# Kernel tuning notes

Hardware: AMD Instinct MI355X
Metric: run time of the kernel (lower is better)

## Reference

```python
import jax, jax.numpy as jnp
import numpy as np
from jax import lax

EPS = 1e-5

def layernorm_c(x, w, b):
    # WithBias LayerNorm over channel dim per spatial location (Restormer style)
    mu = jnp.mean(x, axis=1, keepdims=True)
    var = jnp.var(x, axis=1, keepdims=True)  # population variance (unbiased=False)
    xn = (x - mu) / jnp.sqrt(var + EPS)
    return xn * w[None, :, None, None] + b[None, :, None, None]

def conv1x1(x, w, b):
    # w: (C_out, C_in)
    y = jnp.einsum('bchw,oc->bohw', x, w)
    return y + b[None, :, None, None]

def dwconv3x3(x, w, b):
    # w: (C, 1, 3, 3), depthwise
    y = lax.conv_general_dilated(x, w, window_strides=(1, 1), padding=((1, 1), (1, 1)),
                                 dimension_numbers=('NCHW', 'OIHW', 'NCHW'),
                                 feature_group_count=x.shape[1])
    return y + b[None, :, None, None]

def to_patches(x, p):
    B, C, H, W = x.shape
    x = x.reshape(B, C, H // p, p, W // p, p)
    return x.transpose(0, 1, 2, 4, 3, 5)  # (B,C,h,w,p,p)

def from_patches(x):
    B, C, h, w, p1, p2 = x.shape
    return x.transpose(0, 1, 2, 4, 3, 5).reshape(B, C, h * p1, w * p2)

def setup_inputs() -> dict:
    key = jax.random.key(0)
    ks = jax.random.split(key, 12)
    B, C, H, W = 8, 128, 192, 192
    s = 0.05
    return {
        'x': jax.random.normal(ks[0], (B, C, H, W), jnp.float32),
        'evt': jax.random.normal(ks[1], (B, C, H, W), jnp.float32),
        'ln_img_w': jnp.ones((C,), jnp.float32),
        'ln_img_b': jnp.zeros((C,), jnp.float32),
        'ln_evt_w': jnp.ones((C,), jnp.float32),
        'ln_evt_b': jnp.zeros((C,), jnp.float32),
        'q_w': jax.random.normal(ks[2], (2 * C, C), jnp.float32) * s,
        'q_b': jnp.zeros((2 * C,), jnp.float32),
        'q_dw_w': jax.random.normal(ks[3], (2 * C, 1, 3, 3), jnp.float32) * s,
        'q_dw_b': jnp.zeros((2 * C,), jnp.float32),
        'kv_w': jax.random.normal(ks[4], (4 * C, C), jnp.float32) * s,
        'kv_b': jnp.zeros((4 * C,), jnp.float32),
        'kv_dw_w': jax.random.normal(ks[5], (4 * C, 1, 3, 3), jnp.float32) * s,
        'kv_dw_b': jnp.zeros((4 * C,), jnp.float32),
        'ln_corr_w': jnp.ones((2 * C,), jnp.float32),
        'ln_corr_b': jnp.zeros((2 * C,), jnp.float32),
        'proj_w': jax.random.normal(ks[6], (C, 2 * C), jnp.float32) * s,
        'proj_b': jnp.zeros((C,), jnp.float32),
    }

def reference(x, evt, ln_img_w, ln_img_b, ln_evt_w, ln_evt_b,
              q_w, q_b, q_dw_w, q_dw_b, kv_w, kv_b, kv_dw_w, kv_dw_b,
              ln_corr_w, ln_corr_b, proj_w, proj_b):
    p = 8
    C = x.shape[1]
    xn = layernorm_c(x, ln_img_w, ln_img_b)
    en = layernorm_c(evt, ln_evt_w, ln_evt_b)
    q = dwconv3x3(conv1x1(xn, q_w, q_b), q_dw_w, q_dw_b)          # (B,2C,H,W)
    kv = dwconv3x3(conv1x1(en, kv_w, kv_b), kv_dw_w, kv_dw_b)      # (B,4C,H,W)
    k, v = kv[:, :2 * C], kv[:, 2 * C:]
    q_p = to_patches(q, p)  # (B,2C,h,w,p,p)
    k_p = to_patches(k, p)
    corr = jnp.fft.irfft2(jnp.fft.rfft2(q_p.astype(jnp.float32)) *
                          jnp.fft.rfft2(k_p.astype(jnp.float32)), s=(p, p))
    corr = from_patches(corr)                                      # (B,2C,H,W)
    corr = layernorm_c(corr, ln_corr_w, ln_corr_b)
    return conv1x1(v * corr, proj_w, proj_b)
```

## Files before the change

kernel.cpp:

```cpp
#include <hip/hip_runtime.h>
#include <stdint.h>

#define BATCH 8
#define CIN   128
#define HH    192
#define WW    192
#define HW    (HH*WW)
#define PXB   576
#define CH    2
#define RS    216

typedef _Float16 half_t;
typedef _Float16 f16x8 __attribute__((ext_vector_type(8)));
typedef _Float16 f16x4 __attribute__((ext_vector_type(4)));
typedef _Float16 f16x2 __attribute__((ext_vector_type(2)));
typedef float    f32x4 __attribute__((ext_vector_type(4)));
typedef float    f32x16 __attribute__((ext_vector_type(16)));
typedef unsigned int u32;

__device__ __forceinline__ float DOT2(u32 a, u32 b, float c) {
#if __has_builtin(__builtin_amdgcn_fdot2)
    return __builtin_amdgcn_fdot2(__builtin_bit_cast(f16x2, a),
                                  __builtin_bit_cast(f16x2, b), c, false);
#else
    f16x2 av = __builtin_bit_cast(f16x2, a), bv = __builtin_bit_cast(f16x2, b);
    return c + (float)av[0] * (float)bv[0] + (float)av[1] * (float)bv[1];
#endif
}

#define SMEM_BYTES 52736
#define WSH_OFF    17408
#define MU_OFF     52224

__global__ __launch_bounds__(256)
void wcvt_kernel(const float* __restrict__ qw, const float* __restrict__ kvw,
                 const float* __restrict__ pw, const float* __restrict__ qdw,
                 const float* __restrict__ kvdw, half_t* __restrict__ out)
{
    int q = blockIdx.x * 256 + threadIdx.x;
    if (q >= 34496) return;
    int idx = q * 4;
    const float* src;
    int off;
    if (idx < 32768)       { src = qw;   off = idx; }
    else if (idx < 98304)  { src = kvw;  off = idx - 32768; }
    else if (idx < 131072) { src = pw;   off = idx - 98304; }
    else if (idx < 133376) { src = qdw;  off = idx - 131072; }
    else                   { src = kvdw; off = idx - 133376; }
    float4 v = *(const float4*)&src[off];
    f16x4 o = { (half_t)v.x, (half_t)v.y, (half_t)v.z, (half_t)v.w };
    *(f16x4*)&out[idx] = o;
}

template<int OC>
__global__ __launch_bounds__(256)
void ln_gemm_kernel(const float* __restrict__ x,
                    const float* __restrict__ lnw, const float* __restrict__ lnb,
                    const half_t* __restrict__ wf16, const float* __restrict__ wb,
                    half_t* __restrict__ out)
{
    __shared__ __attribute__((aligned(16))) char smem[SMEM_BYTES];
    half_t (*As)[136]  = (half_t(*)[136])smem;
    half_t (*Wsh)[136] = (half_t(*)[136])(smem + WSH_OFF);
    float  (*Cst)[68]  = (float (*)[68]) (smem + WSH_OFF);
    float* redA = (float*)(smem + WSH_OFF);
    float* redB = (float*)(smem + WSH_OFF + 4096);
    float* mu_s = (float*)(smem + MU_OFF);
    float* rs_s = mu_s + 64;

    const int tid  = threadIdx.x;
    const int l    = tid & 63;
    const int w    = tid >> 6;
    const int lrow = l & 31;
    const int lk   = (l >> 5) * 8;

    const long p0  = (long)blockIdx.x * 64;
    const int  b   = (int)(p0 / HW);
    const int  hw0 = (int)(p0 - (long)b * HW);

    const int pxq = tid & 15;
    const int cg  = tid >> 4;
    const float* xb = x + (size_t)b * CIN * HW + hw0 + pxq * 4;
    float4 vals[8];
    float4 s1 = {0.f,0.f,0.f,0.f}, s2 = {0.f,0.f,0.f,0.f};
#pragma unroll
    for (int j = 0; j < 8; ++j) {
        float4 vv = *(const float4*)&xb[(size_t)(cg * 8 + j) * HW];
        vals[j] = vv;
        s1.x += vv.x; s1.y += vv.y; s1.z += vv.z; s1.w += vv.w;
        s2.x += vv.x*vv.x; s2.y += vv.y*vv.y; s2.z += vv.z*vv.z; s2.w += vv.w*vv.w;
    }
    redA[cg * 64 + pxq * 4 + 0] = s1.x; redB[cg * 64 + pxq * 4 + 0] = s2.x;
    redA[cg * 64 + pxq * 4 + 1] = s1.y; redB[cg * 64 + pxq * 4 + 1] = s2.y;
    redA[cg * 64 + pxq * 4 + 2] = s1.z; redB[cg * 64 + pxq * 4 + 2] = s2.z;
    redA[cg * 64 + pxq * 4 + 3] = s1.w; redB[cg * 64 + pxq * 4 + 3] = s2.w;
    __syncthreads();
    if (tid < 64) {
        float su = 0.f, sq = 0.f;
#pragma unroll
        for (int c = 0; c < 16; ++c) { su += redA[c * 64 + tid]; sq += redB[c * 64 + tid]; }
        float mu  = su * (1.f / 128.f);
        float var = sq * (1.f / 128.f) - mu * mu;
        mu_s[tid] = mu;
        rs_s[tid] = rsqrtf(var + 1e-5f);
    }
    __syncthreads();
    {
        float mu_a[4], rs_a[4];
#pragma unroll
        for (int k = 0; k < 4; ++k) { mu_a[k] = mu_s[pxq * 4 + k]; rs_a[k] = rs_s[pxq * 4 + k]; }
#pragma unroll
        for (int k = 0; k < 4; ++k) {
            f16x8 o;
#pragma unroll
            for (int j = 0; j < 8; ++j) {
                int c = cg * 8 + j;
                float v = (k == 0) ? vals[j].x : (k == 1) ? vals[j].y
                        : (k == 2) ? vals[j].z : vals[j].w;
                o[j] = (half_t)((v - mu_a[k]) * rs_a[k] * lnw[c] + lnb[c]);
            }
            *(f16x8*)&As[pxq * 4 + k][cg * 8] = o;
        }
    }

    for (int nc = 0; nc < OC / 128; ++nc) {
        const int n0 = nc * 128;
        if (nc) __syncthreads();
#pragma unroll
        for (int i = 0; i < 8; ++i) {
            int f  = i * 256 + tid;
            int n  = f >> 4;
            int xh = (f & 15) * 8;
            *(f16x8*)&Wsh[n][xh] = *(const f16x8*)&wf16[(size_t)(n0 + n) * CIN + xh];
        }
        __syncthreads();

        f16x8 af[8];
#pragma unroll
        for (int kk = 0; kk < 8; ++kk)
            af[kk] = *(const f16x8*)&Wsh[w * 32 + lrow][kk * 16 + lk];

        f32x16 acc0, acc1;
#pragma unroll
        for (int i = 0; i < 16; ++i) { acc0[i] = 0.f; acc1[i] = 0.f; }
#pragma unroll
        for (int kk = 0; kk < 8; ++kk) {
            f16x8 b0 = *(const f16x8*)&As[lrow][kk * 16 + lk];
            f16x8 b1 = *(const f16x8*)&As[32 + lrow][kk * 16 + lk];
            acc0 = __builtin_amdgcn_mfma_f32_32x32x16_f16(af[kk], b0, acc0, 0, 0, 0);
            acc1 = __builtin_amdgcn_mfma_f32_32x32x16_f16(af[kk], b1, acc1, 0, 0, 0);
        }
        __syncthreads();

#pragma unroll
        for (int r = 0; r < 16; ++r) {
            int oc = w * 32 + (r & 3) + 8 * (r >> 2) + 4 * (l >> 5);
            Cst[oc][lrow]      = acc0[r];
            Cst[oc][32 + lrow] = acc1[r];
        }
        __syncthreads();

#pragma unroll
        for (int i = 0; i < 4; ++i) {
            int idx = i * 256 + tid;
            int oc  = idx >> 3;
            int pxg = idx & 7;
            const float4 a = *(const float4*)&Cst[oc][pxg * 8];
            const float4 c = *(const float4*)&Cst[oc][pxg * 8 + 4];
            float bias = wb[n0 + oc];
            f16x8 o = { (half_t)(a.x + bias), (half_t)(a.y + bias),
                        (half_t)(a.z + bias), (half_t)(a.w + bias),
                        (half_t)(c.x + bias), (half_t)(c.y + bias),
                        (half_t)(c.z + bias), (half_t)(c.w + bias) };
            *(f16x8*)&out[((size_t)b * OC + n0 + oc) * HW + hw0 + pxg * 8] = o;
        }
    }
}

__global__ __launch_bounds__(256)
void corr_strip_kernel(const half_t* __restrict__ q1, const half_t* __restrict__ kv1,
                       const half_t* __restrict__ qdw16, const float* __restrict__ qb,
                       const half_t* __restrict__ kdw16, const float* __restrict__ kb,
                       half_t* __restrict__ corr, half_t* __restrict__ vd)
{
    __shared__ __attribute__((aligned(16))) half_t raw[6][10][RS];
    __shared__ __attribute__((aligned(16))) half_t qd[2][8][RS];
    __shared__ __attribute__((aligned(16))) half_t krev[2][8][RS];

    const int bid = blockIdx.x;
    const int cg  = bid & 127;
    const int ph  = (bid >> 7) % 24;
    const int lb  = (bid >> 7) / 24;
    const int c0  = cg * CH;
    const int tid = threadIdx.x;

    if (tid < 120) {
        int side = tid & 1;
        int row  = (tid >> 1) % 10;
        int a    = tid / 20;
        f16x8 z = {};
        *(f16x8*)&raw[a][row][side ? 200 : 0] = z;
    }

    for (int i = 0; i < 6; ++i) {
        int idx = tid + 256 * i;
        if (idx >= 1440) break;
        int vec = idx % 24;
        int row = (idx / 24) % 10;
        int a   = idx / 240;
        int ch  = a & 1;
        int gh  = ph * 8 - 1 + row;
        f16x8 v = {};
        if (gh >= 0 && gh < HH) {
            const half_t* src;
            if (a < 2)      src = q1  + ((size_t)lb * 256 + c0 + ch) * HW;
            else if (a < 4) src = kv1 + ((size_t)lb * 512 + c0 + ch) * HW;
            else            src = kv1 + ((size_t)lb * 512 + 256 + c0 + ch) * HW;
            v = *(const f16x8*)&src[(size_t)gh * WW + vec * 8];
        }
        *(f16x8*)&raw[a][row][8 + vec * 8] = v;
    }
    __syncthreads();

    for (int i = 0; i < 3; ++i) {
        int unit = tid + 256 * i;
        if (unit >= 576) break;
        int u   = unit & 7;
        int xg2 = (unit >> 3) % 12;
        int a   = unit / 96;
        int ch  = a & 1;
        const half_t (*rw)[RS] = raw[a];
        const half_t* wt;
        float bias;
        if (a < 2)      { wt = qdw16 + (size_t)(c0 + ch) * 9;       bias = qb[c0 + ch]; }
        else if (a < 4) { wt = kdw16 + (size_t)(c0 + ch) * 9;       bias = kb[c0 + ch]; }
        else            { wt = kdw16 + (size_t)(256 + c0 + ch) * 9; bias = kb[256 + c0 + ch]; }
        u32 w01[3], w2z[3];
#pragma unroll
        for (int dy = 0; dy < 3; ++dy) {
            u32 a0 = (u32)__builtin_bit_cast(unsigned short, wt[dy * 3 + 0]);
            u32 a1 = (u32)__builtin_bit_cast(unsigned short, wt[dy * 3 + 1]);
            u32 a2 = (u32)__builtin_bit_cast(unsigned short, wt[dy * 3 + 2]);
            w01[dy] = a0 | (a1 << 16);
            w2z[dy] = a2;
        }
        const int x0 = xg2 * 16;
        float acc[16];
#pragma unroll
        for (int xx = 0; xx < 16; ++xx) acc[xx] = bias;
#pragma unroll
        for (int dy = 0; dy < 3; ++dy) {
            const half_t* rowp = &rw[u + dy][x0];
            uint4 c0v = *(const uint4*)(rowp);
            uint4 c1v = *(const uint4*)(rowp + 8);
            uint4 c2v = *(const uint4*)(rowp + 16);
            uint4 c3v = *(const uint4*)(rowp + 24);
            u32 H[13] = {c0v.x,c0v.y,c0v.z,c0v.w, c1v.x,c1v.y,c1v.z,c1v.w,
                         c2v.x,c2v.y,c2v.z,c2v.w, c3v.x};
            u32 A[12];
#pragma unroll
            for (int m = 3; m < 12; ++m) A[m] = (H[m] >> 16) | (H[m + 1] << 16);
#pragma unroll
            for (int xx = 0; xx < 16; ++xx) {
                u32 p01 = (xx & 1) ? H[(7 + xx) >> 1] : A[3 + (xx >> 1)];
                u32 p2  = (xx & 1) ? H[(9 + xx) >> 1] : A[4 + (xx >> 1)];
                acc[xx] = DOT2(p01, w01[dy], acc[xx]);
                acc[xx] = DOT2(p2,  w2z[dy], acc[xx]);
            }
        }
        f16x8 o0, o1;
#pragma unroll
        for (int xx = 0; xx < 8; ++xx) { o0[xx] = (half_t)acc[xx]; o1[xx] = (half_t)acc[8 + xx]; }
        if (a < 2) {
            *(f16x8*)&qd[ch][u][x0]     = o0;
            *(f16x8*)&qd[ch][u][x0 + 8] = o1;
        } else if (a < 4) {
            f16x8 r0v, r1v;
            r0v[0] = (half_t)acc[0];
            r1v[0] = (half_t)acc[8];
#pragma unroll
            for (int j = 1; j < 8; ++j) {
                r0v[j] = (half_t)acc[8 - j];
                r1v[j] = (half_t)acc[16 - j];
            }
            *(f16x8*)&krev[ch][u][x0]     = r0v;
            *(f16x8*)&krev[ch][u][x0 + 8] = r1v;
        } else {
            half_t* dst = &vd[((size_t)lb * 256 + c0 + ch) * HW + (size_t)(ph * 8 + u) * WW + x0];
            *(f16x8*)dst       = o0;
            *(f16x8*)(dst + 8) = o1;
        }
    }
    __syncthreads();

    for (int i = 0; i < 2; ++i) {
        int unit = tid + 256 * i;
        if (unit >= 384) break;
        int c   = unit / 192;
        int rem = unit % 192;
        int pw  = rem >> 3;
        int u   = rem & 7;
        float acc[8];
#pragma unroll
        for (int v = 0; v < 8; ++v) acc[v] = 0.f;
#pragma unroll
        for (int s = 0; s < 8; ++s) {
            int r = (u - s) & 7;
            uint4 q4 = *(const uint4*)&qd[c][s][pw * 8];
            uint4 k4 = *(const uint4*)&krev[c][r][pw * 8];
            u32 Q[4] = {q4.x, q4.y, q4.z, q4.w};
            u32 K[4] = {k4.x, k4.y, k4.z, k4.w};
            u32 S[4];
#pragma unroll
            for (int m = 0; m < 4; ++m) S[m] = (K[m] >> 16) | (K[(m + 1) & 3] << 16);
#pragma unroll
            for (int v = 0; v < 8; ++v) {
                const int o = 8 - v;
#pragma unroll
                for (int tt = 0; tt < 4; ++tt) {
                    u32 pr = (o & 1) ? S[(((o - 1) >> 1) + tt) & 3]
                                     : K[((o >> 1) + tt) & 3];
                    acc[v] = DOT2(Q[tt], pr, acc[v]);
                }
            }
        }
        f16x8 ov;
#pragma unroll
        for (int v = 0; v < 8; ++v) ov[v] = (half_t)acc[v];
        *(f16x8*)&corr[((size_t)lb * 256 + c0 + c) * HW + (size_t)(ph * 8 + u) * WW + pw * 8] = ov;
    }
}

__global__ __launch_bounds__(256)
void proj_kernel(const half_t* __restrict__ corr, const half_t* __restrict__ vd,
                 const float* __restrict__ lnw, const float* __restrict__ lnb,
                 const half_t* __restrict__ wp16, const float* __restrict__ wb,
                 float* __restrict__ out)
{
    __shared__ __attribute__((aligned(16))) char smem[SMEM_BYTES];
    half_t (*As)[136]  = (half_t(*)[136])smem;
    half_t (*Wsh)[136] = (half_t(*)[136])(smem + WSH_OFF);
    float  (*Cst)[68]  = (float (*)[68]) (smem + WSH_OFF);
    float* redA = (float*)(smem + WSH_OFF);
    float* redB = (float*)(smem + WSH_OFF + 8192);
    float* mu_s = (float*)(smem + MU_OFF);
    float* rs_s = mu_s + 64;

    const int tid  = threadIdx.x;
    const int l    = tid & 63;
    const int w    = tid >> 6;
    const int lrow = l & 31;
    const int lk   = (l >> 5) * 8;

    const long p0  = (long)blockIdx.x * 64;
    const int  lb  = (int)(p0 / HW);
    const int  hw0 = (int)(p0 - (long)lb * HW);

    const int pxq8 = tid & 7;
    const int cg   = tid >> 3;
    const half_t* cb = corr + (size_t)lb * 256 * HW + hw0 + pxq8 * 8;
    const half_t* vb = vd   + (size_t)lb * 256 * HW + hw0 + pxq8 * 8;

    f16x8 cpk[8];
    float s1[8], s2[8];
#pragma unroll
    for (int p = 0; p < 8; ++p) { s1[p] = 0.f; s2[p] = 0.f; }
#pragma unroll
    for (int j = 0; j < 8; ++j) {
        cpk[j] = *(const f16x8*)&cb[(size_t)(cg * 8 + j) * HW];
#pragma unroll
        for (int p = 0; p < 8; ++p) {
            float f = (float)cpk[j][p];
            s1[p] += f; s2[p] += f * f;
        }
    }
#pragma unroll
    for (int p = 0; p < 8; ++p) {
        redA[cg * 64 + pxq8 * 8 + p] = s1[p];
        redB[cg * 64 + pxq8 * 8 + p] = s2[p];
    }
    __syncthreads();
    if (tid < 64) {
        float su = 0.f, sq = 0.f;
#pragma unroll
        for (int c = 0; c < 32; ++c) { su += redA[c * 64 + tid]; sq += redB[c * 64 + tid]; }
        float mu  = su * (1.f / 256.f);
        float var = sq * (1.f / 256.f) - mu * mu;
        mu_s[tid] = mu;
        rs_s[tid] = rsqrtf(var + 1e-5f);
    }
    __syncthreads();

    f32x16 acc0, acc1;
#pragma unroll
    for (int i = 0; i < 16; ++i) { acc0[i] = 0.f; acc1[i] = 0.f; }

    for (int kc = 0; kc < 2; ++kc) {
        if (kc) __syncthreads();
        if ((cg >> 4) == kc) {
            const int cgl = cg & 15;
            float mu8[8], rs8[8];
#pragma unroll
            for (int p = 0; p < 8; ++p) {
                mu8[p] = mu_s[pxq8 * 8 + p];
                rs8[p] = rs_s[pxq8 * 8 + p];
            }
            f16x8 vvv[8];
            float lw[8], lbv[8];
#pragma unroll
            for (int j = 0; j < 8; ++j) {
                int c = kc * 128 + cgl * 8 + j;
                vvv[j] = *(const f16x8*)&vb[(size_t)c * HW];
                lw[j]  = lnw[c]; lbv[j] = lnb[c];
            }
#pragma unroll
            for (int p = 0; p < 8; ++p) {
                f16x8 o;
#pragma unroll
                for (int j = 0; j < 8; ++j) {
                    float cf = (float)cpk[j][p];
                    o[j] = (half_t)(((cf - mu8[p]) * rs8[p] * lw[j] + lbv[j]) * (float)vvv[j][p]);
                }
                *(f16x8*)&As[pxq8 * 8 + p][cgl * 8] = o;
            }
        }
#pragma unroll
        for (int i = 0; i < 8; ++i) {
            int f  = i * 256 + tid;
            int n  = f >> 4;
            int xh = (f & 15) * 8;
            *(f16x8*)&Wsh[n][xh] = *(const f16x8*)&wp16[(size_t)n * 256 + kc * 128 + xh];
        }
        __syncthreads();

        f16x8 af[8];
#pragma unroll
        for (int kk = 0; kk < 8; ++kk)
            af[kk] = *(const f16x8*)&Wsh[w * 32 + lrow][kk * 16 + lk];
#pragma unroll
        for (int kk = 0; kk < 8; ++kk) {
            f16x8 b0 = *(const f16x8*)&As[lrow][kk * 16 + lk];
            f16x8 b1 = *(const f16x8*)&As[32 + lrow][kk * 16 + lk];
            acc0 = __builtin_amdgcn_mfma_f32_32x32x16_f16(af[kk], b0, acc0, 0, 0, 0);
            acc1 = __builtin_amdgcn_mfma_f32_32x32x16_f16(af[kk], b1, acc1, 0, 0, 0);
        }
    }
    __syncthreads();

#pragma unroll
    for (int r = 0; r < 16; ++r) {
        int oc = w * 32 + (r & 3) + 8 * (r >> 2) + 4 * (l >> 5);
        Cst[oc][lrow]      = acc0[r];
        Cst[oc][32 + lrow] = acc1[r];
    }
    __syncthreads();

#pragma unroll
    for (int i = 0; i < 8; ++i) {
        int idx = i * 256 + tid;
        int oc  = idx >> 4;
        int pxq = idx & 15;
        float4 a = *(const float4*)&Cst[oc][pxq * 4];
        float bias = wb[oc];
        a.x += bias; a.y += bias; a.z += bias; a.w += bias;
        *(float4*)&out[((size_t)lb * 128 + oc) * HW + hw0 + pxq * 4] = a;
    }
}

extern "C" void kernel_launch(void* const* d_in, const int* in_sizes, int n_in,
                              void* d_out, int out_size, void* d_ws, size_t ws_size,
                              hipStream_t stream)
{
    const float* x        = (const float*)d_in[0];
    const float* evt      = (const float*)d_in[1];
    const float* ln_img_w = (const float*)d_in[2];
    const float* ln_img_b = (const float*)d_in[3];
    const float* ln_evt_w = (const float*)d_in[4];
    const float* ln_evt_b = (const float*)d_in[5];
    const float* q_w      = (const float*)d_in[6];
    const float* q_b      = (const float*)d_in[7];
    const float* q_dw_w   = (const float*)d_in[8];
    const float* q_dw_b   = (const float*)d_in[9];
    const float* kv_w     = (const float*)d_in[10];
    const float* kv_b     = (const float*)d_in[11];
    const float* kv_dw_w  = (const float*)d_in[12];
    const float* kv_dw_b  = (const float*)d_in[13];
    const float* ln_corr_w= (const float*)d_in[14];
    const float* ln_corr_b= (const float*)d_in[15];
    const float* proj_w   = (const float*)d_in[16];
    const float* proj_b   = (const float*)d_in[17];
    float* out = (float*)d_out;

    const size_t wtail = (ws_size - 278528) & ~(size_t)255;
    half_t* wf    = (half_t*)((char*)d_ws + wtail);
    half_t* wq16  = wf;
    half_t* wkv16 = wf + 32768;
    half_t* wp16  = wf + 98304;
    half_t* qdw16 = wf + 131072;
    half_t* kdw16 = wf + 133376;

    const size_t per_b = (size_t)(256 + 512 + 256 + 256) * HW * sizeof(half_t);
    int PB = 1;
    if      (wtail >= 8 * per_b) PB = 8;
    else if (wtail >= 4 * per_b) PB = 4;
    else if (wtail >= 2 * per_b) PB = 2;

    half_t* q1   = (half_t*)d_ws;
    half_t* kv1  = q1  + (size_t)PB * 256 * HW;
    half_t* vd   = kv1 + (size_t)PB * 512 * HW;
    half_t* corr = vd  + (size_t)PB * 256 * HW;

    dim3 blk(256);
    wcvt_kernel<<<135, blk, 0, stream>>>(q_w, kv_w, proj_w, q_dw_w, kv_dw_w, wf);

    for (int b0 = 0; b0 < BATCH; b0 += PB) {
        int nb = PB;
        ln_gemm_kernel<256><<<nb * PXB, blk, 0, stream>>>(
            x + (size_t)b0 * CIN * HW, ln_img_w, ln_img_b, wq16, q_b, q1);
        ln_gemm_kernel<512><<<nb * PXB, blk, 0, stream>>>(
            evt + (size_t)b0 * CIN * HW, ln_evt_w, ln_evt_b, wkv16, kv_b, kv1);
        corr_strip_kernel<<<nb * 24 * 128, blk, 0, stream>>>(
            q1, kv1, qdw16, q_dw_b, kdw16, kv_dw_b, corr, vd);
        proj_kernel<<<nb * PXB, blk, 0, stream>>>(
            corr, vd, ln_corr_w, ln_corr_b, wp16, proj_b,
            out + (size_t)b0 * 128 * HW);
    }
}
```

Baseline: 650.9 us.

## Merge q/kv LN-GEMMs and overlap projection with next-chunk LN-GEMM

The two LayerNorm+1x1-conv kernels are refactored into device bodies and launched together as one interleaved-block kernel, so q and kv are computed in a single launch. When the batch is processed in chunks, the projection for the current chunk and the LN-GEMMs for the next chunk are dispatched in the same grid. This is meant to cut launch count and fill the GPU during kernel tails by co-scheduling independent work. In exchange, the LN-GEMM output-channel count becomes a runtime value, which may cost some unrolling, and the heterogeneous blocks can raise register and LDS pressure.

```diff
diff --git a/kernel.cpp b/kernel.cpp
--- a/kernel.cpp
+++ b/kernel.cpp
@@ -52,14 +52,12 @@
     *(f16x4*)&out[idx] = o;
 }
 
-template<int OC>
-__global__ __launch_bounds__(256)
-void ln_gemm_kernel(const float* __restrict__ x,
-                    const float* __restrict__ lnw, const float* __restrict__ lnb,
-                    const half_t* __restrict__ wf16, const float* __restrict__ wb,
-                    half_t* __restrict__ out)
-{
-    __shared__ __attribute__((aligned(16))) char smem[SMEM_BYTES];
+__device__ void ln_gemm_body(char* smem, int bid, int OC,
+    const float* __restrict__ x,
+    const float* __restrict__ lnw, const float* __restrict__ lnb,
+    const half_t* __restrict__ wf16, const float* __restrict__ wb,
+    half_t* __restrict__ out)
+{
     half_t (*As)[136]  = (half_t(*)[136])smem;
     half_t (*Wsh)[136] = (half_t(*)[136])(smem + WSH_OFF);
     float  (*Cst)[68]  = (float (*)[68]) (smem + WSH_OFF);
@@ -74,9 +72,8 @@
     const int lrow = l & 31;
     const int lk   = (l >> 5) * 8;
 
-    const long p0  = (long)blockIdx.x * 64;
-    const int  b   = (int)(p0 / HW);
-    const int  hw0 = (int)(p0 - (long)b * HW);
+    const int b   = bid / PXB;
+    const int hw0 = (bid - b * PXB) * 64;
 
     const int pxq = tid & 15;
     const int cg  = tid >> 4;
@@ -123,7 +120,7 @@
         }
     }
 
-    for (int nc = 0; nc < OC / 128; ++nc) {
+    for (int nc = 0; nc < (OC >> 7); ++nc) {
         const int n0 = nc * 128;
         if (nc) __syncthreads();
 #pragma unroll
@@ -175,6 +172,193 @@
             *(f16x8*)&out[((size_t)b * OC + n0 + oc) * HW + hw0 + pxg * 8] = o;
         }
     }
+}
+
+__device__ void proj_body(char* smem, int bid,
+    const half_t* __restrict__ corr, const half_t* __restrict__ vd,
+    const float* __restrict__ lnw, const float* __restrict__ lnb,
+    const half_t* __restrict__ wp16, const float* __restrict__ wb,
+    float* __restrict__ out)
+{
+    half_t (*As)[136]  = (half_t(*)[136])smem;
+    half_t (*Wsh)[136] = (half_t(*)[136])(smem + WSH_OFF);
+    float  (*Cst)[68]  = (float (*)[68]) (smem + WSH_OFF);
+    float* redA = (float*)(smem + WSH_OFF);
+    float* redB = (float*)(smem + WSH_OFF + 8192);
+    float* mu_s = (float*)(smem + MU_OFF);
+    float* rs_s = mu_s + 64;
+
+    const int tid  = threadIdx.x;
+    const int l    = tid & 63;
+    const int w    = tid >> 6;
+    const int lrow = l & 31;
+    const int lk   = (l >> 5) * 8;
+
+    const int lb  = bid / PXB;
+    const int hw0 = (bid - lb * PXB) * 64;
+
+    const int pxq8 = tid & 7;
+    const int cg   = tid >> 3;
+    const half_t* cb = corr + (size_t)lb * 256 * HW + hw0 + pxq8 * 8;
+    const half_t* vb = vd   + (size_t)lb * 256 * HW + hw0 + pxq8 * 8;
+
+    f16x8 cpk[8];
+    float s1[8], s2[8];
+#pragma unroll
+    for (int p = 0; p < 8; ++p) { s1[p] = 0.f; s2[p] = 0.f; }
+#pragma unroll
+    for (int j = 0; j < 8; ++j) {
+        cpk[j] = *(const f16x8*)&cb[(size_t)(cg * 8 + j) * HW];
+#pragma unroll
+        for (int p = 0; p < 8; ++p) {
+            float f = (float)cpk[j][p];
+            s1[p] += f; s2[p] += f * f;
+        }
+    }
+#pragma unroll
+    for (int p = 0; p < 8; ++p) {
+        redA[cg * 64 + pxq8 * 8 + p] = s1[p];
+        redB[cg * 64 + pxq8 * 8 + p] = s2[p];
+    }
+    __syncthreads();
+    if (tid < 64) {
+        float su = 0.f, sq = 0.f;
+#pragma unroll
+        for (int c = 0; c < 32; ++c) { su += redA[c * 64 + tid]; sq += redB[c * 64 + tid]; }
+        float mu  = su * (1.f / 256.f);
+        float var = sq * (1.f / 256.f) - mu * mu;
+        mu_s[tid] = mu;
+        rs_s[tid] = rsqrtf(var + 1e-5f);
+    }
+    __syncthreads();
+
+    f32x16 acc0, acc1;
+#pragma unroll
+    for (int i = 0; i < 16; ++i) { acc0[i] = 0.f; acc1[i] = 0.f; }
+
+    for (int kc = 0; kc < 2; ++kc) {
+        if (kc) __syncthreads();
+        if ((cg >> 4) == kc) {
+            const int cgl = cg & 15;
+            float mu8[8], rs8[8];
+#pragma unroll
+            for (int p = 0; p < 8; ++p) {
+                mu8[p] = mu_s[pxq8 * 8 + p];
+                rs8[p] = rs_s[pxq8 * 8 + p];
+            }
+            f16x8 vvv[8];
+            float lw[8], lbv[8];
+#pragma unroll
+            for (int j = 0; j < 8; ++j) {
+                int c = kc * 128 + cgl * 8 + j;
+                vvv[j] = *(const f16x8*)&vb[(size_t)c * HW];
+                lw[j]  = lnw[c]; lbv[j] = lnb[c];
+            }
+#pragma unroll
+            for (int p = 0; p < 8; ++p) {
+                f16x8 o;
+#pragma unroll
+                for (int j = 0; j < 8; ++j) {
+                    float cf = (float)cpk[j][p];
+                    o[j] = (half_t)(((cf - mu8[p]) * rs8[p] * lw[j] + lbv[j]) * (float)vvv[j][p]);
+                }
+                *(f16x8*)&As[pxq8 * 8 + p][cgl * 8] = o;
+            }
+        }
+#pragma unroll
+        for (int i = 0; i < 8; ++i) {
+            int f  = i * 256 + tid;
+            int n  = f >> 4;
+            int xh = (f & 15) * 8;
+            *(f16x8*)&Wsh[n][xh] = *(const f16x8*)&wp16[(size_t)n * 256 + kc * 128 + xh];
+        }
+        __syncthreads();
+
+        f16x8 af[8];
+#pragma unroll
+        for (int kk = 0; kk < 8; ++kk)
+            af[kk] = *(const f16x8*)&Wsh[w * 32 + lrow][kk * 16 + lk];
+#pragma unroll
+        for (int kk = 0; kk < 8; ++kk) {
+            f16x8 b0 = *(const f16x8*)&As[lrow][kk * 16 + lk];
+            f16x8 b1 = *(const f16x8*)&As[32 + lrow][kk * 16 + lk];
+            acc0 = __builtin_amdgcn_mfma_f32_32x32x16_f16(af[kk], b0, acc0, 0, 0, 0);
+            acc1 = __builtin_amdgcn_mfma_f32_32x32x16_f16(af[kk], b1, acc1, 0, 0, 0);
+        }
+    }
+    __syncthreads();
+
+#pragma unroll
+    for (int r = 0; r < 16; ++r) {
+        int oc = w * 32 + (r & 3) + 8 * (r >> 2) + 4 * (l >> 5);
+        Cst[oc][lrow]      = acc0[r];
+        Cst[oc][32 + lrow] = acc1[r];
+    }
+    __syncthreads();
+
+#pragma unroll
+    for (int i = 0; i < 8; ++i) {
+        int idx = i * 256 + tid;
+        int oc  = idx >> 4;
+        int pxq = idx & 15;
+        float4 a = *(const float4*)&Cst[oc][pxq * 4];
+        float bias = wb[oc];
+        a.x += bias; a.y += bias; a.z += bias; a.w += bias;
+        *(float4*)&out[((size_t)lb * 128 + oc) * HW + hw0 + pxq * 4] = a;
+    }
+}
+
+__global__ __launch_bounds__(256)
+void ln_pair_kernel(const float* __restrict__ x, const float* __restrict__ evt,
+                    const float* __restrict__ liw, const float* __restrict__ lib,
+                    const float* __restrict__ lew, const float* __restrict__ leb,
+                    const half_t* __restrict__ wq, const float* __restrict__ qb,
+                    const half_t* __restrict__ wkv, const float* __restrict__ kvb,
+                    half_t* __restrict__ q1, half_t* __restrict__ kv1)
+{
+    __shared__ __attribute__((aligned(16))) char smem[SMEM_BYTES];
+    int idx = blockIdx.x >> 1;
+    if ((blockIdx.x & 1) == 0)
+        ln_gemm_body(smem, idx, 256, x,   liw, lib, wq,  qb,  q1);
+    else
+        ln_gemm_body(smem, idx, 512, evt, lew, leb, wkv, kvb, kv1);
+}
+
+__global__ __launch_bounds__(256)
+void proj_ln_kernel(int nbpxb,
+                    const half_t* __restrict__ corr, const half_t* __restrict__ vd,
+                    const float* __restrict__ lcw, const float* __restrict__ lcb,
+                    const half_t* __restrict__ wp, const float* __restrict__ pb,
+                    float* __restrict__ out,
+                    const float* __restrict__ x, const float* __restrict__ evt,
+                    const float* __restrict__ liw, const float* __restrict__ lib,
+                    const float* __restrict__ lew, const float* __restrict__ leb,
+                    const half_t* __restrict__ wq, const float* __restrict__ qb,
+                    const half_t* __restrict__ wkv, const float* __restrict__ kvb,
+                    half_t* __restrict__ q1, half_t* __restrict__ kv1)
+{
+    __shared__ __attribute__((aligned(16))) char smem[SMEM_BYTES];
+    int bid = blockIdx.x;
+    if (bid < nbpxb) {
+        proj_body(smem, bid, corr, vd, lcw, lcb, wp, pb, out);
+    } else {
+        int t   = bid - nbpxb;
+        int idx = t >> 1;
+        if ((t & 1) == 0)
+            ln_gemm_body(smem, idx, 256, x,   liw, lib, wq,  qb,  q1);
+        else
+            ln_gemm_body(smem, idx, 512, evt, lew, leb, wkv, kvb, kv1);
+    }
+}
+
+__global__ __launch_bounds__(256)
+void proj_kernel(const half_t* __restrict__ corr, const half_t* __restrict__ vd,
+                 const float* __restrict__ lnw, const float* __restrict__ lnb,
+                 const half_t* __restrict__ wp16, const float* __restrict__ wb,
+                 float* __restrict__ out)
+{
+    __shared__ __attribute__((aligned(16))) char smem[SMEM_BYTES];
+    proj_body(smem, blockIdx.x, corr, vd, lnw, lnb, wp16, wb, out);
 }
 
 __global__ __launch_bounds__(256)
@@ -328,142 +512,6 @@
 #pragma unroll
         for (int v = 0; v < 8; ++v) ov[v] = (half_t)acc[v];
         *(f16x8*)&corr[((size_t)lb * 256 + c0 + c) * HW + (size_t)(ph * 8 + u) * WW + pw * 8] = ov;
-    }
-}
-
-__global__ __launch_bounds__(256)
-void proj_kernel(const half_t* __restrict__ corr, const half_t* __restrict__ vd,
-                 const float* __restrict__ lnw, const float* __restrict__ lnb,
-                 const half_t* __restrict__ wp16, const float* __restrict__ wb,
-                 float* __restrict__ out)
-{
-    __shared__ __attribute__((aligned(16))) char smem[SMEM_BYTES];
-    half_t (*As)[136]  = (half_t(*)[136])smem;
-    half_t (*Wsh)[136] = (half_t(*)[136])(smem + WSH_OFF);
-    float  (*Cst)[68]  = (float (*)[68]) (smem + WSH_OFF);
-    float* redA = (float*)(smem + WSH_OFF);
-    float* redB = (float*)(smem + WSH_OFF + 8192);
-    float* mu_s = (float*)(smem + MU_OFF);
-    float* rs_s = mu_s + 64;
-
-    const int tid  = threadIdx.x;
-    const int l    = tid & 63;
-    const int w    = tid >> 6;
-    const int lrow = l & 31;
-    const int lk   = (l >> 5) * 8;
-
-    const long p0  = (long)blockIdx.x * 64;
-    const int  lb  = (int)(p0 / HW);
-    const int  hw0 = (int)(p0 - (long)lb * HW);
-
-    const int pxq8 = tid & 7;
-    const int cg   = tid >> 3;
-    const half_t* cb = corr + (size_t)lb * 256 * HW + hw0 + pxq8 * 8;
-    const half_t* vb = vd   + (size_t)lb * 256 * HW + hw0 + pxq8 * 8;
-
-    f16x8 cpk[8];
-    float s1[8], s2[8];
-#pragma unroll
-    for (int p = 0; p < 8; ++p) { s1[p] = 0.f; s2[p] = 0.f; }
-#pragma unroll
-    for (int j = 0; j < 8; ++j) {
-        cpk[j] = *(const f16x8*)&cb[(size_t)(cg * 8 + j) * HW];
-#pragma unroll
-        for (int p = 0; p < 8; ++p) {
-            float f = (float)cpk[j][p];
-            s1[p] += f; s2[p] += f * f;
-        }
-    }
-#pragma unroll
-    for (int p = 0; p < 8; ++p) {
-        redA[cg * 64 + pxq8 * 8 + p] = s1[p];
-        redB[cg * 64 + pxq8 * 8 + p] = s2[p];
-    }
-    __syncthreads();
-    if (tid < 64) {
-        float su = 0.f, sq = 0.f;
-#pragma unroll
-        for (int c = 0; c < 32; ++c) { su += redA[c * 64 + tid]; sq += redB[c * 64 + tid]; }
-        float mu  = su * (1.f / 256.f);
-        float var = sq * (1.f / 256.f) - mu * mu;
-        mu_s[tid] = mu;
-        rs_s[tid] = rsqrtf(var + 1e-5f);
-    }
-    __syncthreads();
-
-    f32x16 acc0, acc1;
-#pragma unroll
-    for (int i = 0; i < 16; ++i) { acc0[i] = 0.f; acc1[i] = 0.f; }
-
-    for (int kc = 0; kc < 2; ++kc) {
-        if (kc) __syncthreads();
-        if ((cg >> 4) == kc) {
-            const int cgl = cg & 15;
-            float mu8[8], rs8[8];
-#pragma unroll
-            for (int p = 0; p < 8; ++p) {
-                mu8[p] = mu_s[pxq8 * 8 + p];
-                rs8[p] = rs_s[pxq8 * 8 + p];
-            }
-            f16x8 vvv[8];
-            float lw[8], lbv[8];
-#pragma unroll
-            for (int j = 0; j < 8; ++j) {
-                int c = kc * 128 + cgl * 8 + j;
-                vvv[j] = *(const f16x8*)&vb[(size_t)c * HW];
-                lw[j]  = lnw[c]; lbv[j] = lnb[c];
-            }
-#pragma unroll
-            for (int p = 0; p < 8; ++p) {
-                f16x8 o;
-#pragma unroll
-                for (int j = 0; j < 8; ++j) {
-                    float cf = (float)cpk[j][p];
-                    o[j] = (half_t)(((cf - mu8[p]) * rs8[p] * lw[j] + lbv[j]) * (float)vvv[j][p]);
-                }
-                *(f16x8*)&As[pxq8 * 8 + p][cgl * 8] = o;
-            }
-        }
-#pragma unroll
-        for (int i = 0; i < 8; ++i) {
-            int f  = i * 256 + tid;
-            int n  = f >> 4;
-            int xh = (f & 15) * 8;
-            *(f16x8*)&Wsh[n][xh] = *(const f16x8*)&wp16[(size_t)n * 256 + kc * 128 + xh];
-        }
-        __syncthreads();
-
-        f16x8 af[8];
-#pragma unroll
-        for (int kk = 0; kk < 8; ++kk)
-            af[kk] = *(const f16x8*)&Wsh[w * 32 + lrow][kk * 16 + lk];
-#pragma unroll
-        for (int kk = 0; kk < 8; ++kk) {
-            f16x8 b0 = *(const f16x8*)&As[lrow][kk * 16 + lk];
-            f16x8 b1 = *(const f16x8*)&As[32 + lrow][kk * 16 + lk];
-            acc0 = __builtin_amdgcn_mfma_f32_32x32x16_f16(af[kk], b0, acc0, 0, 0, 0);
-            acc1 = __builtin_amdgcn_mfma_f32_32x32x16_f16(af[kk], b1, acc1, 0, 0, 0);
-        }
-    }
-    __syncthreads();
-
-#pragma unroll
-    for (int r = 0; r < 16; ++r) {
-        int oc = w * 32 + (r & 3) + 8 * (r >> 2) + 4 * (l >> 5);
-        Cst[oc][lrow]      = acc0[r];
-        Cst[oc][32 + lrow] = acc1[r];
-    }
-    __syncthreads();
-
-#pragma unroll
-    for (int i = 0; i < 8; ++i) {
-        int idx = i * 256 + tid;
-        int oc  = idx >> 4;
-        int pxq = idx & 15;
-        float4 a = *(const float4*)&Cst[oc][pxq * 4];
-        float bias = wb[oc];
-        a.x += bias; a.y += bias; a.z += bias; a.w += bias;
-        *(float4*)&out[((size_t)lb * 128 + oc) * HW + hw0 + pxq * 4] = a;
     }
 }
 
@@ -513,16 +561,26 @@
     dim3 blk(256);
     wcvt_kernel<<<135, blk, 0, stream>>>(q_w, kv_w, proj_w, q_dw_w, kv_dw_w, wf);
 
+    ln_pair_kernel<<<2 * PB * PXB, blk, 0, stream>>>(
+        x, evt, ln_img_w, ln_img_b, ln_evt_w, ln_evt_b,
+        wq16, q_b, wkv16, kv_b, q1, kv1);
+
     for (int b0 = 0; b0 < BATCH; b0 += PB) {
-        int nb = PB;
-        ln_gemm_kernel<256><<<nb * PXB, blk, 0, stream>>>(
-            x + (size_t)b0 * CIN * HW, ln_img_w, ln_img_b, wq16, q_b, q1);
-        ln_gemm_kernel<512><<<nb * PXB, blk, 0, stream>>>(
-            evt + (size_t)b0 * CIN * HW, ln_evt_w, ln_evt_b, wkv16, kv_b, kv1);
-        corr_strip_kernel<<<nb * 24 * 128, blk, 0, stream>>>(
+        corr_strip_kernel<<<PB * 24 * 128, blk, 0, stream>>>(
             q1, kv1, qdw16, q_dw_b, kdw16, kv_dw_b, corr, vd);
-        proj_kernel<<<nb * PXB, blk, 0, stream>>>(
-            corr, vd, ln_corr_w, ln_corr_b, wp16, proj_b,
-            out + (size_t)b0 * 128 * HW);
-    }
-}
+        if (b0 + PB < BATCH) {
+            const float* xn = x   + (size_t)(b0 + PB) * CIN * HW;
+            const float* en = evt + (size_t)(b0 + PB) * CIN * HW;
+            proj_ln_kernel<<<3 * PB * PXB, blk, 0, stream>>>(
+                PB * PXB,
+                corr, vd, ln_corr_w, ln_corr_b, wp16, proj_b,
+                out + (size_t)b0 * 128 * HW,
+                xn, en, ln_img_w, ln_img_b, ln_evt_w, ln_evt_b,
+                wq16, q_b, wkv16, kv_b, q1, kv1);
+        } else {
+            proj_kernel<<<PB * PXB, blk, 0, stream>>>(
+                corr, vd, ln_corr_w, ln_corr_b, wp16, proj_b,
+                out + (size_t)b0 * 128 * HW);
+        }
+    }
+}
```

New measurement: 1.034 ms. 58.9% more time.
